# Kernel tuning notes

Measured on AMD Instinct MI355X. Metric: run time of the kernel, lower is better.

The kernel has to match this reference:

```python
import jax, jax.numpy as jnp
import numpy as np

N_FFT = 512
HOP = 128
WIN = 512
LENGTH = 600  # hardcoded in the original forward


def _hann(n):
    # torch.hann_window default is periodic: 0.5*(1-cos(2*pi*i/n))
    i = jnp.arange(n, dtype=jnp.float32)
    return 0.5 * (1.0 - jnp.cos(2.0 * jnp.pi * i / n))


def setup_inputs() -> dict:
    key = jax.random.key(0)
    x = jax.random.normal(key, (8192, 1, 257, 6, 2), dtype=jnp.float32)
    return {"x": x}


def reference(x):
    B, C, F, T, D = x.shape  # C==1, F==n_fft//2+1, D==2
    # view(B, F, T, D) + view_as_complex
    spec = x[:, 0, :, :, 0] + 1j * x[:, 0, :, :, 1]          # [B, F, T] complex64
    # inverse real FFT per frame (torch.istft, normalized=False, onesided=True)
    frames = jnp.fft.irfft(spec.transpose(0, 2, 1), n=N_FFT, axis=-1)  # [B, T, n_fft]
    win = _hann(WIN)                                          # [n_fft] (win_length == n_fft)
    frames = frames * win                                     # synthesis windowing
    # overlap-add
    L = HOP * (T - 1) + N_FFT
    idx = jnp.arange(T)[:, None] * HOP + jnp.arange(N_FFT)[None, :]  # [T, n_fft]
    y = jnp.zeros((B, L), dtype=frames.dtype).at[:, idx].add(frames)  # [B, L]
    # window-square envelope normalization (COLA division)
    env = jnp.zeros((L,), dtype=frames.dtype).at[idx].add(win * win)  # [L]
    # center=True trim of n_fft//2, then length=600 crop
    start = N_FFT // 2
    sig = y[:, start:start + LENGTH] / env[start:start + LENGTH]       # [B, 600]
    return sig[:, None, :]                                    # unsqueeze(1) -> [B, 1, 600]
```

## Files before the change

### kernel.cpp

```cpp
#include <hip/hip_runtime.h>
#include <hip/hip_bf16.h>


#define NFFT   512
#define HOP    128
#define KDIM   3084
#define KP     3136
#define NOUT   600
#define NP     640
#define BM     64
#define BN     128
#define BK     64
#define KSTEPS (KP / BK)
#define LDA    72

typedef short s16x8 __attribute__((ext_vector_type(8)));
typedef float f32x4 __attribute__((ext_vector_type(4)));

static __device__ __forceinline__ unsigned short bf16_bits(float f) {
    __hip_bfloat16 b = __float2bfloat16(f);
    return *(unsigned short*)&b;
}

__global__ __launch_bounds__(256) void gen_W(unsigned short* __restrict__ Wt) {
    __shared__ float costab[512];
    __shared__ __align__(16) unsigned short rowbuf[KP];
    const int l   = blockIdx.x;
    const int tid = threadIdx.x;
    const float w0 = 6.283185307179586f / 512.0f;

    *(int4*)(rowbuf + tid * 8) = make_int4(0, 0, 0, 0);
    if (tid < 136) *(int4*)(rowbuf + (256 + tid) * 8) = make_int4(0, 0, 0, 0);
    costab[tid]       = __cosf((float)tid * w0);
    costab[tid + 256] = __cosf((float)(tid + 256) * w0);
    __syncthreads();

    if (l < NOUT) {
        const int p = l + 256;
        float env = 0.0f;
#pragma unroll
        for (int tt = 0; tt < 6; ++tt) {
            int m = p - HOP * tt;
            if (m >= 0 && m < NFFT) {
                float w = 0.5f - 0.5f * costab[m];
                env += w * w;
            }
        }
        const float inv = 1.0f / (512.0f * env);
        for (int f = tid; f <= 256; f += 256) {
            float cf = (f == 0 || f == 256) ? 1.0f : 2.0f;
#pragma unroll
            for (int t = 0; t < 6; ++t) {
                int n = p - HOP * t;
                if (n >= 0 && n < NFFT) {
                    float w = 0.5f - 0.5f * costab[n];
                    float scale = cf * w * inv;
                    int a = (f * n) & 511;
                    float c = costab[a];
                    float s = costab[(a + 384) & 511];
                    rowbuf[f * 12 + t * 2 + 0] = bf16_bits(scale * c);
                    rowbuf[f * 12 + t * 2 + 1] = bf16_bits(-scale * s);
                }
            }
        }
    }
    __syncthreads();

    unsigned short* dst = Wt + (size_t)l * KP;
    *(int4*)(dst + tid * 8) = *(const int4*)(rowbuf + tid * 8);
    if (tid < 136) *(int4*)(dst + (256 + tid) * 8) = *(const int4*)(rowbuf + (256 + tid) * 8);
}

__global__ __launch_bounds__(256, 5) void gemm_kernel(
        const float* __restrict__ X,
        const unsigned short* __restrict__ Wt,
        float* __restrict__ out) {
    __shared__ __align__(16) unsigned short As[BM * LDA];
    __shared__ __align__(16) unsigned short Bs[BN * LDA];

    const int tid = threadIdx.x;
    const int bid  = blockIdx.x;
    const int xcd  = bid & 7;
    const int rest = bid >> 3;
    const int mt   = xcd * 16 + rest / 10;
    const int sub  = rest % 10;
    const int nt   = sub >> 1;
    const int kidx = sub & 1;
    const int mBase = mt * BM;
    const int nBase = nt * BN;
    const int sBeg  = kidx ? 25 : 0;
    const int sEnd  = kidx ? KSTEPS : 25;

    const int lane = tid & 63;
    const int wave = tid >> 6;
    const int wm   = (wave & 1) * 32;
    const int wn   = (wave >> 1) * 64;
    const int lrow = lane & 15;
    const int quad = lane >> 4;

    const int aRow = tid >> 4, aU = tid & 15;
    const int bRow = tid >> 3, bU = tid & 7;
    const float* aPtr = X + (size_t)(mBase + aRow) * KDIM + sBeg * BK + aU * 4;
    const unsigned short* bPtr = Wt + (size_t)(nBase + bRow) * KP + sBeg * BK + bU * 8;
    const int aColBase = aU * 4;
    const size_t aRowStride = (size_t)16 * KDIM;
    const size_t bRowStride = (size_t)32 * KP;

    f32x4 acc[2][4];
#pragma unroll
    for (int i = 0; i < 2; ++i)
#pragma unroll
        for (int j = 0; j < 4; ++j) acc[i][j] = (f32x4){0.f, 0.f, 0.f, 0.f};

    float4 av[4];
    s16x8  bv[4];
    {
        const int k0 = sBeg * BK;
#pragma unroll
        for (int p = 0; p < 4; ++p) {
            av[p] = make_float4(0.f, 0.f, 0.f, 0.f);
            if (k0 + aColBase < KDIM) av[p] = *(const float4*)(aPtr + p * aRowStride);
            bv[p] = *(const s16x8*)(const void*)(bPtr + p * bRowStride);
        }
    }

    for (int step = sBeg; step < sEnd; ++step) {
#pragma unroll
        for (int p = 0; p < 4; ++p) {
            float4 v = av[p];
            unsigned long long pk = (unsigned long long)bf16_bits(v.x) |
                                    ((unsigned long long)bf16_bits(v.y) << 16) |
                                    ((unsigned long long)bf16_bits(v.z) << 32) |
                                    ((unsigned long long)bf16_bits(v.w) << 48);
            *(unsigned long long*)(As + (aRow + 16 * p) * LDA + aU * 4) = pk;
            *(s16x8*)(void*)(Bs + (bRow + 32 * p) * LDA + bU * 8) = bv[p];
        }
        __syncthreads();

        if (step + 1 < sEnd) {
            const int k0 = (step + 1) * BK;
#pragma unroll
            for (int p = 0; p < 4; ++p) {
                av[p] = make_float4(0.f, 0.f, 0.f, 0.f);
                if (k0 + aColBase < KDIM)
                    av[p] = *(const float4*)(aPtr + (size_t)(step + 1 - sBeg) * BK + p * aRowStride);
                bv[p] = *(const s16x8*)(const void*)(bPtr + (size_t)(step + 1 - sBeg) * BK + p * bRowStride);
            }
        }

#pragma unroll
        for (int ks = 0; ks < 2; ++ks) {
            const int koff = ks * 32 + quad * 8;
            s16x8 bfr[4];
#pragma unroll
            for (int j = 0; j < 4; ++j)
                bfr[j] = *(const s16x8*)(const void*)(Bs + (wn + j * 16 + lrow) * LDA + koff);
#pragma unroll
            for (int i = 0; i < 2; ++i) {
                s16x8 afr = *(const s16x8*)(const void*)(As + (wm + i * 16 + lrow) * LDA + koff);
#pragma unroll
                for (int j = 0; j < 4; ++j)
                    acc[i][j] = __builtin_amdgcn_mfma_f32_16x16x32_bf16(
                        afr, bfr[j], acc[i][j], 0, 0, 0);
            }
        }
        __syncthreads();
    }

#pragma unroll
    for (int i = 0; i < 2; ++i) {
#pragma unroll
        for (int j = 0; j < 4; ++j) {
            int gn = nBase + wn + j * 16 + lrow;
            if (gn < NOUT) {
#pragma unroll
                for (int r = 0; r < 4; ++r) {
                    int gm = mBase + wm + i * 16 + quad * 4 + r;
                    atomicAdd(out + (size_t)gm * NOUT + gn, acc[i][j][r]);
                }
            }
        }
    }
}

extern "C" void kernel_launch(void* const* d_in, const int* in_sizes, int n_in,
                              void* d_out, int out_size, void* d_ws, size_t ws_size,
                              hipStream_t stream) {
    const float* X = (const float*)d_in[0];
    unsigned short* W = (unsigned short*)d_ws;
    float* out = (float*)d_out;

    hipMemsetAsync(d_out, 0, (size_t)out_size * sizeof(float), stream);
    gen_W<<<dim3(NP), 256, 0, stream>>>(W);
    gemm_kernel<<<dim3(128 * 5 * 2), 256, 0, stream>>>(X, W, out);
}
```

Measured before the change: 240.9 us.

## Prefetch A tiles two steps ahead with register double-buffering in GEMM loop

The GEMM main loop is unrolled by two, and the fp32 A-tile loads now come from two register buffers, so A is fetched two K-steps ahead instead of one. __syncthreads is replaced by an LDS-only barrier that waits only on lgkmcnt rather than on outstanding global loads, letting global prefetches stay in flight across barriers. The aim is to hide global load latency better. In exchange, register pressure rises and launch bounds drop from 5 to 4 waves per SIMD, reducing occupancy.

New measurement: 232.7 us. 1.03x faster.

```diff
diff --git a/kernel.cpp b/kernel.cpp
--- a/kernel.cpp
+++ b/kernel.cpp
@@ -20,6 +20,12 @@
 static __device__ __forceinline__ unsigned short bf16_bits(float f) {
     __hip_bfloat16 b = __float2bfloat16(f);
     return *(unsigned short*)&b;
+}
+
+static __device__ __forceinline__ void lds_barrier() {
+    asm volatile("s_waitcnt lgkmcnt(0)" ::: "memory");
+    __builtin_amdgcn_s_barrier();
+    asm volatile("" ::: "memory");
 }
 
 __global__ __launch_bounds__(256) void gen_W(unsigned short* __restrict__ Wt) {
@@ -71,7 +77,7 @@
     if (tid < 136) *(int4*)(dst + (256 + tid) * 8) = *(const int4*)(rowbuf + (256 + tid) * 8);
 }
 
-__global__ __launch_bounds__(256, 5) void gemm_kernel(
+__global__ __launch_bounds__(256, 4) void gemm_kernel(
         const float* __restrict__ X,
         const unsigned short* __restrict__ Wt,
         float* __restrict__ out) {
@@ -112,60 +118,90 @@
 #pragma unroll
         for (int j = 0; j < 4; ++j) acc[i][j] = (f32x4){0.f, 0.f, 0.f, 0.f};
 
-    float4 av[4];
+#define ISSUE_A(AV, s)                                                         \
+    {                                                                          \
+        const int k0_ = (s) * BK;                                              \
+        _Pragma("unroll")                                                      \
+        for (int p = 0; p < 4; ++p) {                                          \
+            AV[p] = make_float4(0.f, 0.f, 0.f, 0.f);                           \
+            if (k0_ + aColBase < KDIM)                                         \
+                AV[p] = *(const float4*)(aPtr + (size_t)((s) - sBeg) * BK +    \
+                                         p * aRowStride);                      \
+        }                                                                      \
+    }
+
+#define ISSUE_B(BV, s)                                                         \
+    {                                                                          \
+        _Pragma("unroll")                                                      \
+        for (int p = 0; p < 4; ++p)                                            \
+            BV[p] = *(const s16x8*)(const void*)(bPtr +                        \
+                        (size_t)((s) - sBeg) * BK + p * bRowStride);           \
+    }
+
+#define STAGE_WRITE(AV, BV)                                                    \
+    {                                                                          \
+        _Pragma("unroll")                                                      \
+        for (int p = 0; p < 4; ++p) {                                          \
+            float4 v = AV[p];                                                  \
+            unsigned long long pk = (unsigned long long)bf16_bits(v.x) |       \
+                                    ((unsigned long long)bf16_bits(v.y) << 16) |\
+                                    ((unsigned long long)bf16_bits(v.z) << 32) |\
+                                    ((unsigned long long)bf16_bits(v.w) << 48); \
+            *(unsigned long long*)(As + (aRow + 16 * p) * LDA + aU * 4) = pk;  \
+            *(s16x8*)(void*)(Bs + (bRow + 32 * p) * LDA + bU * 8) = BV[p];     \
+        }                                                                      \
+    }
+
+#define COMPUTE()                                                              \
+    {                                                                          \
+        _Pragma("unroll")                                                      \
+        for (int ks = 0; ks < 2; ++ks) {                                       \
+            const int koff = ks * 32 + quad * 8;                               \
+            s16x8 bfr[4];                                                      \
+            _Pragma("unroll")                                                  \
+            for (int j = 0; j < 4; ++j)                                        \
+                bfr[j] = *(const s16x8*)(const void*)(Bs +                     \
+                             (wn + j * 16 + lrow) * LDA + koff);               \
+            _Pragma("unroll")                                                  \
+            for (int i = 0; i < 2; ++i) {                                      \
+                s16x8 afr = *(const s16x8*)(const void*)(As +                  \
+                                (wm + i * 16 + lrow) * LDA + koff);            \
+                _Pragma("unroll")                                              \
+                for (int j = 0; j < 4; ++j)                                    \
+                    acc[i][j] = __builtin_amdgcn_mfma_f32_16x16x32_bf16(       \
+                        afr, bfr[j], acc[i][j], 0, 0, 0);                      \
+            }                                                                  \
+        }                                                                      \
+    }
+
+    float4 av0[4], av1[4];
     s16x8  bv[4];
-    {
-        const int k0 = sBeg * BK;
-#pragma unroll
-        for (int p = 0; p < 4; ++p) {
-            av[p] = make_float4(0.f, 0.f, 0.f, 0.f);
-            if (k0 + aColBase < KDIM) av[p] = *(const float4*)(aPtr + p * aRowStride);
-            bv[p] = *(const s16x8*)(const void*)(bPtr + p * bRowStride);
-        }
-    }
-
-    for (int step = sBeg; step < sEnd; ++step) {
-#pragma unroll
-        for (int p = 0; p < 4; ++p) {
-            float4 v = av[p];
-            unsigned long long pk = (unsigned long long)bf16_bits(v.x) |
-                                    ((unsigned long long)bf16_bits(v.y) << 16) |
-                                    ((unsigned long long)bf16_bits(v.z) << 32) |
-                                    ((unsigned long long)bf16_bits(v.w) << 48);
-            *(unsigned long long*)(As + (aRow + 16 * p) * LDA + aU * 4) = pk;
-            *(s16x8*)(void*)(Bs + (bRow + 32 * p) * LDA + bU * 8) = bv[p];
-        }
-        __syncthreads();
+    ISSUE_A(av0, sBeg);
+    ISSUE_A(av1, sBeg + 1);
+    ISSUE_B(bv, sBeg);
+
+    for (int step = sBeg; step < sEnd; step += 2) {
+        STAGE_WRITE(av0, bv);
+        if (step + 1 < sEnd) ISSUE_B(bv, step + 1);
+        if (step + 2 < sEnd) ISSUE_A(av0, step + 2);
+        lds_barrier();
+        COMPUTE();
+        lds_barrier();
 
         if (step + 1 < sEnd) {
-            const int k0 = (step + 1) * BK;
-#pragma unroll
-            for (int p = 0; p < 4; ++p) {
-                av[p] = make_float4(0.f, 0.f, 0.f, 0.f);
-                if (k0 + aColBase < KDIM)
-                    av[p] = *(const float4*)(aPtr + (size_t)(step + 1 - sBeg) * BK + p * aRowStride);
-                bv[p] = *(const s16x8*)(const void*)(bPtr + (size_t)(step + 1 - sBeg) * BK + p * bRowStride);
-            }
-        }
-
-#pragma unroll
-        for (int ks = 0; ks < 2; ++ks) {
-            const int koff = ks * 32 + quad * 8;
-            s16x8 bfr[4];
-#pragma unroll
-            for (int j = 0; j < 4; ++j)
-                bfr[j] = *(const s16x8*)(const void*)(Bs + (wn + j * 16 + lrow) * LDA + koff);
-#pragma unroll
-            for (int i = 0; i < 2; ++i) {
-                s16x8 afr = *(const s16x8*)(const void*)(As + (wm + i * 16 + lrow) * LDA + koff);
-#pragma unroll
-                for (int j = 0; j < 4; ++j)
-                    acc[i][j] = __builtin_amdgcn_mfma_f32_16x16x32_bf16(
-                        afr, bfr[j], acc[i][j], 0, 0, 0);
-            }
-        }
-        __syncthreads();
-    }
+            STAGE_WRITE(av1, bv);
+            if (step + 2 < sEnd) ISSUE_B(bv, step + 2);
+            if (step + 3 < sEnd) ISSUE_A(av1, step + 3);
+            lds_barrier();
+            COMPUTE();
+            lds_barrier();
+        }
+    }
+
+#undef ISSUE_A
+#undef ISSUE_B
+#undef STAGE_WRITE
+#undef COMPUTE
 
 #pragma unroll
     for (int i = 0; i < 2; ++i) {
```
